# Kernel tuning notes

Measured on AMD Instinct MI355X. Metric: run time of the kernel, lower is better.

## Reference

```python
import jax, jax.numpy as jnp
import numpy as np

N_ENT, N_CON, DIM, R, NB = 30000, 29309, 128, 12, 8
B, LC, S, E_DB, E_CON = 256, 50, 32, 300000, 200000


def setup_inputs() -> dict:
    key = jax.random.key(0)
    ks = jax.random.split(key, 32)
    f = lambda k, sh: (jax.random.normal(k, sh, jnp.float32) * 0.02)
    concept_emb = f(ks[0], (N_CON, DIM)).at[0].set(0.0)  # padding_idx=0 row zeroed
    inp = {
        'concept_mask': jax.random.randint(ks[1], (B, LC), 0, N_CON, jnp.int32),
        'seed_pad': jax.random.randint(ks[2], (B, S), 0, N_ENT, jnp.int32),
        'seed_lens': jax.random.randint(ks[3], (B,), 0, S + 1, jnp.int32),
        'db_edge_index': jax.random.randint(ks[4], (2, E_DB), 0, N_ENT, jnp.int32),
        'db_edge_type': jax.random.randint(ks[5], (E_DB,), 0, R, jnp.int32),
        'con_edge_index': jax.random.randint(ks[6], (2, E_CON), 0, N_CON, jnp.int32),
        'db_vec': jax.random.uniform(ks[7], (B, N_ENT), jnp.float32),
        'labels': jax.random.randint(ks[8], (B,), 0, N_ENT, jnp.int64),
        'rec': jax.random.uniform(ks[9], (B,), jnp.float32),
        'concept_emb': concept_emb,
        'basis': f(ks[10], (NB, N_ENT, DIM)),
        'comp': f(ks[11], (R, NB)),
        'rgcn_root': f(ks[12], (N_ENT, DIM)),
        'rgcn_bias': jnp.zeros((DIM,), jnp.float32),
        'gcn_w': f(ks[13], (DIM, DIM)),
        'gcn_b': jnp.zeros((DIM,), jnp.float32),
        'attn_a': f(ks[14], (DIM, DIM)),
        'attn_b': f(ks[15], (DIM, 1)),
        'attn_a_db': f(ks[16], (DIM, DIM)),
        'attn_b_db': f(ks[17], (DIM, 1)),
        'user_norm_w': f(ks[18], (DIM, 2 * DIM)),
        'user_norm_b': jnp.zeros((DIM,), jnp.float32),
        'gate_norm_w': f(ks[19], (1, DIM)),
        'gate_norm_b': jnp.zeros((1,), jnp.float32),
        'info_con_w': f(ks[20], (DIM, DIM)),
        'info_con_b': jnp.zeros((DIM,), jnp.float32),
        'info_out_db_b': jnp.zeros((N_ENT,), jnp.float32),
        'output_en_b': jnp.zeros((N_ENT,), jnp.float32),
    }
    return inp


def _forward(concept_mask, seed_pad, seed_lens, db_edge_index, db_edge_type,
             con_edge_index, db_vec, labels, rec, concept_emb, basis, comp,
             rgcn_root, rgcn_bias, gcn_w, gcn_b, attn_a, attn_b, attn_a_db,
             attn_b_db, user_norm_w, user_norm_b, gate_norm_w, gate_norm_b,
             info_con_w, info_con_b, info_out_db_b, output_en_b):
    NEG = jnp.float32(-1e30)
    # ---- RGCN over DBpedia graph (x=None -> per-edge row W[rel][src]) ----
    w = jnp.einsum('rb,bnd->rnd', comp, basis)            # [R, N_ent, D]
    src, dst = db_edge_index[0], db_edge_index[1]
    msg = w[db_edge_type, src]                            # [E, D]
    agg = jax.ops.segment_sum(msg, dst, num_segments=N_ENT)
    cnt = jax.ops.segment_sum(jnp.ones_like(dst, jnp.float32), dst, num_segments=N_ENT)
    db_feats = agg / jnp.maximum(cnt, 1.0)[:, None] + rgcn_root + rgcn_bias  # mean aggr + root + bias
    # ---- GCN over concept graph (symmetric norm, self-loops) ----
    xw = concept_emb @ gcn_w
    loops = jnp.arange(N_CON, dtype=con_edge_index.dtype)
    cs = jnp.concatenate([con_edge_index[0], loops])
    cd = jnp.concatenate([con_edge_index[1], loops])
    deg = jax.ops.segment_sum(jnp.ones_like(cd, jnp.float32), cd, num_segments=N_CON)
    dinv = jnp.where(deg > 0, jax.lax.rsqrt(jnp.maximum(deg, 1e-12)), 0.0)
    norm = dinv[cs] * dinv[cd]
    con_feats = jax.ops.segment_sum(norm[:, None] * xw[cs], cd, num_segments=N_CON) + gcn_b
    # ---- per-sample seed-set self-attention over db features ----
    h = db_feats[seed_pad]                                # [B, S, D]
    e = jnp.tanh(h @ attn_a_db) @ attn_b_db               # [B, S, 1]
    valid = jnp.arange(S)[None, :] < seed_lens[:, None]   # [B, S]
    a = jax.nn.softmax(jnp.where(valid[..., None], e, NEG), axis=1)
    db_user = jnp.einsum('bso,bsd->bd', a, h)             # weighted sum (o=1)
    has_seed = (seed_lens > 0)
    db_user = jnp.where(has_seed[:, None], db_user, 0.0)  # empty seed set -> zeros
    db_con_mask = has_seed.astype(jnp.float32)
    # ---- batch self-attention over gathered concept features ----
    hc = con_feats[concept_mask]                          # [B, LC, D]
    ec = jnp.tanh(hc @ attn_a) @ attn_b                   # [B, LC, 1]
    cvalid = (concept_mask != 0)
    ac = jax.nn.softmax(jnp.where(cvalid[..., None], ec, NEG), axis=1)
    con_user = jnp.einsum('blo,bld->bd', ac, hc)
    # ---- gated fusion ----
    u = jnp.concatenate([con_user, db_user], axis=-1) @ user_norm_w.T + user_norm_b
    gate = jax.nn.sigmoid(u @ gate_norm_w.T + gate_norm_b)  # [B, 1]
    user_emb = gate * db_user + (1.0 - gate) * con_user
    entity_scores = user_emb @ db_feats.T + output_en_b   # [B, N_ent]
    # ---- infomax MSE loss ----
    con_e = con_user @ info_con_w.T + info_con_b
    db_scores = con_e @ db_feats.T + info_out_db_b
    info_db_loss = jnp.mean(jnp.sum((db_scores - db_vec) ** 2, axis=-1) * db_con_mask)
    # ---- rec CE loss ----
    logp = jax.nn.log_softmax(entity_scores, axis=-1)
    ce = -jnp.take_along_axis(logp, labels[:, None].astype(jnp.int32), axis=1)[:, 0]
    rec_loss = jnp.sum(ce * rec)
    loss = rec_loss + 0.025 * info_db_loss                # pretrain=False path
    return loss, entity_scores, rec_loss


def reference(concept_mask, seed_pad, seed_lens, db_edge_index, db_edge_type,
              con_edge_index, db_vec, labels, rec, concept_emb, basis, comp,
              rgcn_root, rgcn_bias, gcn_w, gcn_b, attn_a, attn_b, attn_a_db,
              attn_b_db, user_norm_w, user_norm_b, gate_norm_w, gate_norm_b,
              info_con_w, info_con_b, info_out_db_b, output_en_b):
    return _forward(concept_mask, seed_pad, seed_lens, db_edge_index, db_edge_type,
                    con_edge_index, db_vec, labels, rec, concept_emb, basis, comp,
                    rgcn_root, rgcn_bias, gcn_w, gcn_b, attn_a, attn_b, attn_a_db,
                    attn_b_db, user_norm_w, user_norm_b, gate_norm_w, gate_norm_b,
                    info_con_w, info_con_b, info_out_db_b, output_en_b)
```

## Files before the change

kernel.cpp:

```cpp
#include <hip/hip_runtime.h>

#define N_ENT  30000
#define N_CON  29309
#define DIM    128
#define NBASIS 8
#define NREL   12
#define BATCH  256
#define LCON   50
#define SSEED  32
#define EDB    300000
#define ECON   200000
#define NTILE  938

#define NE4      ((N_CON * DIM) / 4)
#define NB_HIST  ((EDB + ECON + 255) / 256)
#define NB_CONV  ((NE4 + (DIM*DIM/4) + 255) / 256)
#define NB_WCOMP ((N_ENT * 32) / 256)
#define NB_GXW   ((N_CON + 31) / 32)
#define NB_RG    ((N_ENT + 3) / 4)
#define NB_GG    ((N_CON + 3) / 4)

typedef __attribute__((ext_vector_type(8)))  short bfrag8;
typedef __attribute__((ext_vector_type(16))) float facc16;

__device__ __forceinline__ unsigned short f2bf(float f) {
    unsigned int u = __float_as_uint(f);
    u += 0x7FFFu + ((u >> 16) & 1u);
    return (unsigned short)(u >> 16);
}
__device__ __forceinline__ float bf2f(unsigned int h) {
    return __uint_as_float(h << 16);
}

__global__ __launch_bounds__(256) void prep_kernel(const int* __restrict__ db_dst,
                                                   const int* __restrict__ con_dst,
                                                   const float* __restrict__ emb,
                                                   const float* __restrict__ W,
                                                   int* __restrict__ cnt_e, int* __restrict__ cnt_c,
                                                   int* __restrict__ ord_db, int* __restrict__ ord_con,
                                                   unsigned short* __restrict__ emb_h,
                                                   unsigned short* __restrict__ Wt_h) {
    int t = threadIdx.x, bb = blockIdx.x;
    if (bb < NB_HIST) {
        int e = bb * 256 + t;
        if (e < EDB) {
            ord_db[e] = atomicAdd(cnt_e + db_dst[e], 1);
        } else if (e < EDB + ECON) {
            int ee = e - EDB;
            ord_con[ee] = atomicAdd(cnt_c + con_dst[ee], 1);
        }
    } else {
        int i = (bb - NB_HIST) * 256 + t;
        if (i < NE4) {
            float4 v = ((const float4*)emb)[i];
            unsigned int p0 = (unsigned int)f2bf(v.x) | ((unsigned int)f2bf(v.y) << 16);
            unsigned int p1 = (unsigned int)f2bf(v.z) | ((unsigned int)f2bf(v.w) << 16);
            *(uint2*)(emb_h + (size_t)i * 4) = make_uint2(p0, p1);
        } else {
            int j = i - NE4;
            if (j < (DIM * DIM) / 4) {
                int o = j * 4;
                int n = o >> 7, k0 = o & 127;
                unsigned int p0 = (unsigned int)f2bf(W[(k0 + 0) * DIM + n]) |
                                  ((unsigned int)f2bf(W[(k0 + 1) * DIM + n]) << 16);
                unsigned int p1 = (unsigned int)f2bf(W[(k0 + 2) * DIM + n]) |
                                  ((unsigned int)f2bf(W[(k0 + 3) * DIM + n]) << 16);
                *(uint2*)(Wt_h + n * DIM + k0) = make_uint2(p0, p1);
            }
        }
    }
}

__device__ void scan_block(const int* __restrict__ cnt, int n, int* __restrict__ rowptr) {
    __shared__ int part[1024];
    int t = threadIdx.x;
    int per = (n + 1023) / 1024;
    int s0 = t * per;
    int sum = 0;
    for (int i = 0; i < per; ++i) {
        int idx = s0 + i;
        if (idx < n) sum += cnt[idx];
    }
    part[t] = sum;
    __syncthreads();
    for (int off = 1; off < 1024; off <<= 1) {
        int v = (t >= off) ? part[t - off] : 0;
        __syncthreads();
        part[t] += v;
        __syncthreads();
    }
    int run = part[t] - sum;
    for (int i = 0; i < per; ++i) {
        int idx = s0 + i;
        if (idx < n) {
            rowptr[idx] = run;
            run += cnt[idx];
        }
    }
    if (t == 1023) rowptr[n] = part[1023];
}

__global__ __launch_bounds__(1024) void scan2_kernel(const int* __restrict__ cnt_e,
                                                     const int* __restrict__ cnt_c,
                                                     int* __restrict__ rowptr_e,
                                                     int* __restrict__ rowptr_c,
                                                     float* __restrict__ dinv) {
    if (blockIdx.x == 0) {
        scan_block(cnt_e, N_ENT, rowptr_e);
    } else {
        scan_block(cnt_c, N_CON, rowptr_c);
        for (int i = threadIdx.x; i < N_CON; i += 1024)
            dinv[i] = rsqrtf((float)(cnt_c[i] + 1));
    }
}

__global__ __launch_bounds__(256) void mid_kernel(const int* __restrict__ db_eidx,
                                                  const int* __restrict__ db_etype,
                                                  const int* __restrict__ con_eidx,
                                                  const int* __restrict__ ord_db,
                                                  const int* __restrict__ ord_con,
                                                  const int* __restrict__ rowptr_e,
                                                  const int* __restrict__ rowptr_c,
                                                  int* __restrict__ elist_e,
                                                  int* __restrict__ elist_c,
                                                  const float* __restrict__ basis,
                                                  const float* __restrict__ comp,
                                                  unsigned short* __restrict__ w_h,
                                                  const unsigned short* __restrict__ emb_h,
                                                  const unsigned short* __restrict__ Wt_h,
                                                  unsigned short* __restrict__ xw_h,
                                                  int use_w) {
    __shared__ float sc[NREL * NBASIS];
    int t = threadIdx.x, bb = blockIdx.x;
    if (bb < NB_HIST) {
        int e = bb * 256 + t;
        if (e < EDB) {
            int dst = db_eidx[EDB + e];
            elist_e[rowptr_e[dst] + ord_db[e]] = db_eidx[e] | (db_etype[e] << 18);
        } else if (e < EDB + ECON) {
            int ee = e - EDB;
            int dst = con_eidx[ECON + ee];
            elist_c[rowptr_c[dst] + ord_con[ee]] = con_eidx[ee];
        }
        return;
    }
    if (bb < NB_HIST + NB_WCOMP) {
        if (!use_w) return;
        if (t < NREL * NBASIS) sc[t] = comp[t];
        __syncthreads();
        int i = (bb - NB_HIST) * 256 + t;
        int n = i >> 5, d4 = i & 31;
        float4 bv[NBASIS];
#pragma unroll
        for (int b = 0; b < NBASIS; ++b)
            bv[b] = ((const float4*)(basis + ((size_t)b * N_ENT + n) * DIM))[d4];
#pragma unroll
        for (int r = 0; r < NREL; ++r) {
            float4 acc = make_float4(0.f, 0.f, 0.f, 0.f);
#pragma unroll
            for (int b = 0; b < NBASIS; ++b) {
                float c = sc[r * NBASIS + b];
                acc.x += c * bv[b].x; acc.y += c * bv[b].y;
                acc.z += c * bv[b].z; acc.w += c * bv[b].w;
            }
            unsigned int p0 = (unsigned int)f2bf(acc.x) | ((unsigned int)f2bf(acc.y) << 16);
            unsigned int p1 = (unsigned int)f2bf(acc.z) | ((unsigned int)f2bf(acc.w) << 16);
            *(uint2*)(w_h + ((size_t)r * N_ENT + n) * DIM + d4 * 4) = make_uint2(p0, p1);
        }
        return;
    }
    {
        int gb = bb - NB_HIST - NB_WCOMP;
        int wave = t >> 6, lane = t & 63;
        int m0 = gb * 32;
        int n0 = wave * 32;
        int am = lane & 31, ak = (lane >> 5) * 8;
        int mrow = m0 + am;
        bool mv = mrow < N_CON;
        const unsigned short* Ar = emb_h + (size_t)mrow * DIM + ak;
        const unsigned short* Br = Wt_h + (size_t)(n0 + am) * DIM + ak;
        facc16 acc;
#pragma unroll
        for (int r = 0; r < 16; ++r) acc[r] = 0.f;
#pragma unroll
        for (int s = 0; s < 8; ++s) {
            bfrag8 a;
#pragma unroll
            for (int j = 0; j < 8; ++j) a[j] = 0;
            if (mv) a = *(const bfrag8*)(Ar + s * 16);
            bfrag8 b = *(const bfrag8*)(Br + s * 16);
            acc = __builtin_amdgcn_mfma_f32_32x32x16_bf16(a, b, acc, 0, 0, 0);
        }
        int col = lane & 31;
        int g4 = (lane >> 5) * 4;
#pragma unroll
        for (int r = 0; r < 16; ++r) {
            int m = m0 + (r & 3) + ((r >> 2) << 3) + g4;
            if (m < N_CON) xw_h[(size_t)m * DIM + n0 + col] = f2bf(acc[r]);
        }
    }
}

__global__ __launch_bounds__(256) void gathers_kernel(const int* __restrict__ rowptr_e,
                                                      const int* __restrict__ elist_e,
                                                      const unsigned short* __restrict__ w_h,
                                                      const float* __restrict__ root,
                                                      const float* __restrict__ bias,
                                                      unsigned short* __restrict__ dbf_h,
                                                      const int* __restrict__ rowptr_c,
                                                      const int* __restrict__ elist_c,
                                                      const float* __restrict__ dinv,
                                                      const unsigned short* __restrict__ xw_h,
                                                      const float* __restrict__ gcn_b,
                                                      unsigned short* __restrict__ conf_h) {
    int bb = blockIdx.x;
    int lane = threadIdx.x & 63;
    if (bb < NB_RG) {
        int wid = bb * 4 + (threadIdx.x >> 6);
        if (wid >= N_ENT) return;
        int beg = rowptr_e[wid], end = rowptr_e[wid + 1];
        float a0 = 0.f, a1 = 0.f;
        int p = beg;
        for (; p + 1 < end; p += 2) {
            int v0 = elist_e[p], v1 = elist_e[p + 1];
            unsigned int k0 = *(const unsigned int*)(w_h + ((size_t)(v0 >> 18) * N_ENT + (v0 & 0x3FFFF)) * DIM + lane * 2);
            unsigned int k1 = *(const unsigned int*)(w_h + ((size_t)(v1 >> 18) * N_ENT + (v1 & 0x3FFFF)) * DIM + lane * 2);
            a0 += bf2f(k0 & 0xFFFF) + bf2f(k1 & 0xFFFF);
            a1 += bf2f(k0 >> 16)    + bf2f(k1 >> 16);
        }
        if (p < end) {
            int v = elist_e[p];
            unsigned int k = *(const unsigned int*)(w_h + ((size_t)(v >> 18) * N_ENT + (v & 0x3FFFF)) * DIM + lane * 2);
            a0 += bf2f(k & 0xFFFF);
            a1 += bf2f(k >> 16);
        }
        float inv = 1.f / fmaxf((float)(end - beg), 1.f);
        size_t base = (size_t)wid * DIM + lane * 2;
        float f0 = a0 * inv + root[base]     + bias[lane * 2];
        float f1 = a1 * inv + root[base + 1] + bias[lane * 2 + 1];
        *(unsigned int*)(dbf_h + base) = (unsigned int)f2bf(f0) | ((unsigned int)f2bf(f1) << 16);
    } else {
        int wid = (bb - NB_RG) * 4 + (threadIdx.x >> 6);
        if (wid >= N_CON) return;
        int beg = rowptr_c[wid], end = rowptr_c[wid + 1];
        float a0 = 0.f, a1 = 0.f;
        int p = beg;
        for (; p + 1 < end; p += 2) {
            int s0 = elist_c[p], s1 = elist_c[p + 1];
            float n0 = dinv[s0], n1 = dinv[s1];
            unsigned int k0 = *(const unsigned int*)(xw_h + (size_t)s0 * DIM + lane * 2);
            unsigned int k1 = *(const unsigned int*)(xw_h + (size_t)s1 * DIM + lane * 2);
            a0 += n0 * bf2f(k0 & 0xFFFF) + n1 * bf2f(k1 & 0xFFFF);
            a1 += n0 * bf2f(k0 >> 16)    + n1 * bf2f(k1 >> 16);
        }
        if (p < end) {
            int s = elist_c[p];
            float nm = dinv[s];
            unsigned int k = *(const unsigned int*)(xw_h + (size_t)s * DIM + lane * 2);
            a0 += nm * bf2f(k & 0xFFFF);
            a1 += nm * bf2f(k >> 16);
        }
        float dv = dinv[wid];
        unsigned int ks = *(const unsigned int*)(xw_h + (size_t)wid * DIM + lane * 2);
        size_t base = (size_t)wid * DIM + lane * 2;
        float f0 = dv * a0 + dv * dv * bf2f(ks & 0xFFFF) + gcn_b[lane * 2];
        float f1 = dv * a1 + dv * dv * bf2f(ks >> 16)    + gcn_b[lane * 2 + 1];
        *(unsigned int*)(conf_h + base) = (unsigned int)f2bf(f0) | ((unsigned int)f2bf(f1) << 16);
    }
}

__global__ __launch_bounds__(256) void rgcn_gather_basis(const int* __restrict__ rowptr,
                                                         const int* __restrict__ elist,
                                                         const float* __restrict__ basis,
                                                         const float* __restrict__ comp,
                                                         const float* __restrict__ root,
                                                         const float* __restrict__ bias,
                                                         unsigned short* __restrict__ dbf_h) {
    int wid  = blockIdx.x * 4 + (threadIdx.x >> 6);
    int lane = threadIdx.x & 63;
    if (wid >= N_ENT) return;
    int beg = rowptr[wid], end = rowptr[wid + 1];
    float a0 = 0.f, a1 = 0.f;
    for (int p = beg; p < end; ++p) {
        int v = elist[p];
        int src = v & 0x3FFFF, ty = v >> 18;
        const float* c = comp + ty * NBASIS;
#pragma unroll
        for (int b = 0; b < NBASIS; ++b) {
            const float* bp = basis + ((size_t)b * N_ENT + src) * DIM;
            a0 += c[b] * bp[lane * 2];
            a1 += c[b] * bp[lane * 2 + 1];
        }
    }
    float inv = 1.f / fmaxf((float)(end - beg), 1.f);
    size_t base = (size_t)wid * DIM + lane * 2;
    float f0 = a0 * inv + root[base]     + bias[lane * 2];
    float f1 = a1 * inv + root[base + 1] + bias[lane * 2 + 1];
    *(unsigned int*)(dbf_h + base) = (unsigned int)f2bf(f0) | ((unsigned int)f2bf(f1) << 16);
}

__device__ void attn_phase(const unsigned short* __restrict__ feats_h,
                           const int* __restrict__ row,
                           const float* __restrict__ A,
                           const float* __restrict__ vvec,
                           float* __restrict__ h, float* __restrict__ sc,
                           float* __restrict__ outv, int S, int len, int mode) {
    int t = threadIdx.x;
    for (int i = t; i < S * (DIM / 2); i += 256) {
        int s = i >> 6, d2 = (i & 63) * 2;
        unsigned int k = *(const unsigned int*)(feats_h + (size_t)row[s] * DIM + d2);
        h[(s << 7) + d2]     = bf2f(k & 0xFFFF);
        h[(s << 7) + d2 + 1] = bf2f(k >> 16);
    }
    if (t < S) sc[t] = 0.f;
    __syncthreads();
    for (int sd = t; sd < S * DIM; sd += 256) {
        int s = sd >> 7, d = sd & 127;
        float acc = 0.f;
        for (int k = 0; k < DIM; ++k) acc += h[(s << 7) + k] * A[(k << 7) + d];
        atomicAdd(&sc[s], tanhf(acc) * vvec[d]);
    }
    __syncthreads();
    if (t == 0) {
        float m = -1e30f;
        for (int s = 0; s < S; ++s) {
            bool valid = (mode == 0) ? (s < len) : (row[s] != 0);
            float e = valid ? sc[s] : -1e30f;
            sc[s] = e;
            m = fmaxf(m, e);
        }
        float sum = 0.f;
        for (int s = 0; s < S; ++s) { float p = __expf(sc[s] - m); sum += p; sc[s] = p; }
        float inv = 1.f / sum;
        for (int s = 0; s < S; ++s) sc[s] *= inv;
    }
    __syncthreads();
    if (t < DIM) {
        float acc = 0.f;
        for (int s = 0; s < S; ++s) acc += sc[s] * h[(s << 7) + t];
        if (mode == 0 && len == 0) acc = 0.f;
        outv[t] = acc;
    }
    __syncthreads();
}

__global__ __launch_bounds__(256) void attn_fusion_kernel(const unsigned short* __restrict__ dbf_h,
                                                          const unsigned short* __restrict__ conf_h,
                                                          const int* __restrict__ seed_pad,
                                                          const int* __restrict__ seed_lens,
                                                          const int* __restrict__ concept_mask,
                                                          const float* __restrict__ A_db, const float* __restrict__ v_db,
                                                          const float* __restrict__ A_c,  const float* __restrict__ v_c,
                                                          const float* __restrict__ Wu, const float* __restrict__ bu,
                                                          const float* __restrict__ gw, const float* __restrict__ gb,
                                                          const float* __restrict__ Wi, const float* __restrict__ bi,
                                                          unsigned short* __restrict__ uemb_h,
                                                          unsigned short* __restrict__ cone_h,
                                                          float* __restrict__ maskv) {
    __shared__ float h[LCON * DIM];
    __shared__ float sc[LCON];
    __shared__ float du[DIM], cu[DIM], red[DIM];
    int b = blockIdx.x, t = threadIdx.x;
    int len = seed_lens[b];
    attn_phase(dbf_h, seed_pad + b * SSEED, A_db, v_db, h, sc, du, SSEED, len, 0);
    attn_phase(conf_h, concept_mask + b * LCON, A_c, v_c, h, sc, cu, LCON, 0, 1);
    if (t < DIM) {
        float u = bu[t];
        const float* wr = Wu + t * 2 * DIM;
        for (int k = 0; k < DIM; ++k) u += cu[k] * wr[k];
        for (int k = 0; k < DIM; ++k) u += du[k] * wr[DIM + k];
        red[t] = u * gw[t];
    }
    __syncthreads();
    for (int s2 = 64; s2 > 0; s2 >>= 1) {
        if (t < s2) red[t] += red[t + s2];
        __syncthreads();
    }
    if (t < DIM) {
        float gate = 1.f / (1.f + __expf(-(red[0] + gb[0])));
        uemb_h[b * DIM + t] = f2bf(gate * du[t] + (1.f - gate) * cu[t]);
        float ce = bi[t];
        const float* wi = Wi + t * DIM;
        for (int k = 0; k < DIM; ++k) ce += cu[k] * wi[k];
        cone_h[b * DIM + t] = f2bf(ce);
    }
    if (t == 0) maskv[b] = (len > 0) ? 1.f : 0.f;
}

__global__ __launch_bounds__(256) void score_mfma(const unsigned short* __restrict__ dbf_h,
                                                  const unsigned short* __restrict__ uemb_h,
                                                  const unsigned short* __restrict__ cone_h,
                                                  const float* __restrict__ en_b,
                                                  const float* __restrict__ info_b,
                                                  const float* __restrict__ db_vec,
                                                  float* __restrict__ escore,
                                                  float* __restrict__ partM,
                                                  float* __restrict__ partS,
                                                  float* __restrict__ partQ) {
    int wave = threadIdx.x >> 6, lane = threadIdx.x & 63;
    int nt = blockIdx.x * 4 + wave;
    if (nt >= NTILE) return;
    int b0 = blockIdx.y * 32;
    int n0 = nt * 32;
    int am = lane & 31, ak = (lane >> 5) * 8;
    int nb = n0 + am;
    bool bvalid = nb < N_ENT;
    const unsigned short* Au = uemb_h + (size_t)(b0 + am) * DIM + ak;
    const unsigned short* Ac = cone_h + (size_t)(b0 + am) * DIM + ak;
    const unsigned short* Bp = dbf_h + (size_t)nb * DIM + ak;
    facc16 accE, accD;
#pragma unroll
    for (int r = 0; r < 16; ++r) { accE[r] = 0.f; accD[r] = 0.f; }
#pragma unroll
    for (int s = 0; s < 8; ++s) {
        bfrag8 au = *(const bfrag8*)(Au + s * 16);
        bfrag8 ac = *(const bfrag8*)(Ac + s * 16);
        bfrag8 bb;
#pragma unroll
        for (int j = 0; j < 8; ++j) bb[j] = 0;
        if (bvalid) bb = *(const bfrag8*)(Bp + s * 16);
        accE = __builtin_amdgcn_mfma_f32_32x32x16_bf16(au, bb, accE, 0, 0, 0);
        accD = __builtin_amdgcn_mfma_f32_32x32x16_bf16(ac, bb, accD, 0, 0, 0);
    }
    int col = lane & 31;
    int n = n0 + col;
    bool nv = n < N_ENT;
    float enb = nv ? en_b[n] : 0.f;
    float inb = nv ? info_b[n] : 0.f;
    int g4 = (lane >> 5) * 4;
#pragma unroll
    for (int r = 0; r < 16; ++r) {
        int b = b0 + (r & 3) + ((r >> 2) << 3) + g4;
        float e = accE[r] + enb;
        if (nv) escore[(size_t)b * N_ENT + n] = e;
        float ev = nv ? e : -1e30f;
        float mx = ev;
#pragma unroll
        for (int off = 16; off >= 1; off >>= 1) mx = fmaxf(mx, __shfl_xor(mx, off, 64));
        float ex = nv ? __expf(e - mx) : 0.f;
        float sm = ex;
#pragma unroll
        for (int off = 16; off >= 1; off >>= 1) sm += __shfl_xor(sm, off, 64);
        float d = nv ? (accD[r] + inb - db_vec[(size_t)b * N_ENT + n]) : 0.f;
        float q = d * d;
#pragma unroll
        for (int off = 16; off >= 1; off >>= 1) q += __shfl_xor(q, off, 64);
        if (col == 0) {
            partM[(size_t)b * NTILE + nt] = mx;
            partS[(size_t)b * NTILE + nt] = sm;
            partQ[(size_t)b * NTILE + nt] = q;
        }
    }
}

__global__ __launch_bounds__(256) void ce_final(const float* __restrict__ partM,
                                                const float* __restrict__ partS,
                                                const float* __restrict__ partQ,
                                                const float* __restrict__ escore,
                                                const int* __restrict__ labels,
                                                const float* __restrict__ rec,
                                                float* __restrict__ rloss,
                                                float* __restrict__ ssqv) {
    __shared__ float red[256], red2[256];
    int b = blockIdx.x, t = threadIdx.x;
    const float* pm = partM + (size_t)b * NTILE;
    const float* ps = partS + (size_t)b * NTILE;
    const float* pq = partQ + (size_t)b * NTILE;
    float mx = -1e30f;
    for (int i = t; i < NTILE; i += 256) mx = fmaxf(mx, pm[i]);
    red[t] = mx;
    __syncthreads();
    for (int s2 = 128; s2 > 0; s2 >>= 1) {
        if (t < s2) red[t] = fmaxf(red[t], red[t + s2]);
        __syncthreads();
    }
    float M = red[0];
    __syncthreads();
    float s = 0.f, q = 0.f;
    for (int i = t; i < NTILE; i += 256) {
        s += ps[i] * __expf(pm[i] - M);
        q += pq[i];
    }
    red[t] = s; red2[t] = q;
    __syncthreads();
    for (int s2 = 128; s2 > 0; s2 >>= 1) {
        if (t < s2) { red[t] += red[t + s2]; red2[t] += red2[t + s2]; }
        __syncthreads();
    }
    if (t == 0) {
        float lse = M + logf(red[0]);
        float ce  = -(escore[(size_t)b * N_ENT + labels[b]] - lse);
        rloss[b]  = ce * rec[b];
        ssqv[b]   = red2[0];
    }
}

__global__ __launch_bounds__(256) void final_kernel(const float* __restrict__ rloss,
                                                    const float* __restrict__ sumsq,
                                                    const float* __restrict__ maskv,
                                                    float* __restrict__ out) {
    __shared__ float r1[256], r2[256];
    int t = threadIdx.x;
    r1[t] = rloss[t];
    r2[t] = sumsq[t] * maskv[t];
    __syncthreads();
    for (int s2 = 128; s2 > 0; s2 >>= 1) {
        if (t < s2) { r1[t] += r1[t + s2]; r2[t] += r2[t + s2]; }
        __syncthreads();
    }
    if (t == 0) {
        float rec_loss = r1[0];
        float info = r2[0] / (float)BATCH;
        out[0] = rec_loss + 0.025f * info;
        out[1 + (size_t)BATCH * N_ENT] = rec_loss;
    }
}

extern "C" void kernel_launch(void* const* d_in, const int* in_sizes, int n_in,
                              void* d_out, int out_size, void* d_ws, size_t ws_size,
                              hipStream_t stream) {
    (void)in_sizes; (void)n_in; (void)out_size;
    const int*   concept_mask  = (const int*)d_in[0];
    const int*   seed_pad      = (const int*)d_in[1];
    const int*   seed_lens     = (const int*)d_in[2];
    const int*   db_eidx       = (const int*)d_in[3];
    const int*   db_etype      = (const int*)d_in[4];
    const int*   con_eidx      = (const int*)d_in[5];
    const float* db_vec        = (const float*)d_in[6];
    const int*   labels        = (const int*)d_in[7];
    const float* rec           = (const float*)d_in[8];
    const float* concept_emb   = (const float*)d_in[9];
    const float* basis         = (const float*)d_in[10];
    const float* comp          = (const float*)d_in[11];
    const float* rgcn_root     = (const float*)d_in[12];
    const float* rgcn_bias     = (const float*)d_in[13];
    const float* gcn_w         = (const float*)d_in[14];
    const float* gcn_b         = (const float*)d_in[15];
    const float* attn_a        = (const float*)d_in[16];
    const float* attn_b        = (const float*)d_in[17];
    const float* attn_a_db     = (const float*)d_in[18];
    const float* attn_b_db     = (const float*)d_in[19];
    const float* user_norm_w   = (const float*)d_in[20];
    const float* user_norm_b   = (const float*)d_in[21];
    const float* gate_norm_w   = (const float*)d_in[22];
    const float* gate_norm_b   = (const float*)d_in[23];
    const float* info_con_w    = (const float*)d_in[24];
    const float* info_con_b    = (const float*)d_in[25];
    const float* info_out_db_b = (const float*)d_in[26];
    const float* output_en_b   = (const float*)d_in[27];

    float* ws = (float*)d_ws;
    size_t off = 0;
    auto alloc = [&](size_t n) { float* p = ws + off; off += (n + 255) & ~(size_t)255; return p; };
    float* dinv   = alloc(N_CON);
    float* maskv  = alloc(BATCH);
    float* rls    = alloc(BATCH);
    float* ssqv   = alloc(BATCH);
    float* partM  = alloc((size_t)BATCH * NTILE);
    float* partS  = alloc((size_t)BATCH * NTILE);
    float* partQ  = alloc((size_t)BATCH * NTILE);
    int* cnt_e    = (int*)alloc(N_ENT + N_CON);
    int* cnt_c    = cnt_e + N_ENT;
    int* rowptr_e = (int*)alloc(N_ENT + 1);
    int* rowptr_c = (int*)alloc(N_CON + 1);
    int* ord_db   = (int*)alloc(EDB);
    int* ord_con  = (int*)alloc(ECON);
    int* elist_e  = (int*)alloc(EDB);
    int* elist_c  = (int*)alloc(ECON);
    unsigned short* dbf_h  = (unsigned short*)alloc((size_t)N_ENT * DIM / 2);
    unsigned short* conf_h = (unsigned short*)alloc((size_t)N_CON * DIM / 2 + 128);
    unsigned short* xw_h   = (unsigned short*)alloc((size_t)N_CON * DIM / 2 + 128);
    unsigned short* emb_h  = (unsigned short*)alloc((size_t)N_CON * DIM / 2 + 128);
    unsigned short* Wt_h   = (unsigned short*)alloc(DIM * DIM / 2);
    unsigned short* uemb_h = (unsigned short*)alloc(BATCH * DIM / 2);
    unsigned short* cone_h = (unsigned short*)alloc(BATCH * DIM / 2);
    size_t w_elems = ((size_t)NREL * N_ENT * DIM) / 2;
    int use_w = (off + w_elems) * sizeof(float) <= ws_size;
    unsigned short* w_h = (unsigned short*)(ws + off);

    float* out    = (float*)d_out;
    float* escore = out + 1;

    (void)hipMemsetAsync(cnt_e, 0, (N_ENT + N_CON) * sizeof(int), stream);

    prep_kernel<<<NB_HIST + NB_CONV, 256, 0, stream>>>(db_eidx + EDB, con_eidx + ECON,
                                                       concept_emb, gcn_w,
                                                       cnt_e, cnt_c, ord_db, ord_con, emb_h, Wt_h);
    scan2_kernel<<<2, 1024, 0, stream>>>(cnt_e, cnt_c, rowptr_e, rowptr_c, dinv);
    mid_kernel<<<NB_HIST + NB_WCOMP + NB_GXW, 256, 0, stream>>>(db_eidx, db_etype, con_eidx,
                                                                ord_db, ord_con, rowptr_e, rowptr_c,
                                                                elist_e, elist_c, basis, comp, w_h,
                                                                emb_h, Wt_h, xw_h, use_w);
    gathers_kernel<<<NB_RG + NB_GG, 256, 0, stream>>>(rowptr_e, elist_e, w_h, rgcn_root, rgcn_bias,
                                                      dbf_h, rowptr_c, elist_c, dinv, xw_h, gcn_b, conf_h);
    if (!use_w) {
        rgcn_gather_basis<<<NB_RG, 256, 0, stream>>>(rowptr_e, elist_e, basis, comp,
                                                     rgcn_root, rgcn_bias, dbf_h);
    }
    attn_fusion_kernel<<<BATCH, 256, 0, stream>>>(dbf_h, conf_h, seed_pad, seed_lens, concept_mask,
                                                  attn_a_db, attn_b_db, attn_a, attn_b,
                                                  user_norm_w, user_norm_b, gate_norm_w, gate_norm_b,
                                                  info_con_w, info_con_b, uemb_h, cone_h, maskv);
    dim3 sg((NTILE + 3) / 4, BATCH / 32);
    score_mfma<<<sg, 256, 0, stream>>>(dbf_h, uemb_h, cone_h, output_en_b, info_out_db_b, db_vec,
                                       escore, partM, partS, partQ);
    ce_final<<<BATCH, 256, 0, stream>>>(partM, partS, partQ, escore, labels, rec, rls, ssqv);
    final_kernel<<<1, 256, 0, stream>>>(rls, ssqv, maskv, out);
}
```

Measured before the change: 591.7 us.

## Precompute per-entity attention scores with MFMA and simplify attention fusion to gathers

The attention logit tanh(h·A)·v depends only on the entity row, not on the batch. It is now computed once for every entity and concept row in a new bf16 MFMA kernel, instead of being recomputed per batch element with scalar FP32 loops over 32 and 50 gathered rows. The attention-fusion kernel then only gathers these scalar scores, runs a wave-level softmax, and does the weighted sum. This removes the per-batch serial matmul and atomics. In exchange it computes scores for all ~59k rows whether or not they are referenced, and it uses bf16 inputs for the attention matrices.

```diff
diff --git a/kernel.cpp b/kernel.cpp
--- a/kernel.cpp
+++ b/kernel.cpp
@@ -14,11 +14,13 @@
 
 #define NE4      ((N_CON * DIM) / 4)
 #define NB_HIST  ((EDB + ECON + 255) / 256)
-#define NB_CONV  ((NE4 + (DIM*DIM/4) + 255) / 256)
+#define NB_CONV  ((NE4 + 3 * (DIM * DIM / 4) + 255) / 256)
 #define NB_WCOMP ((N_ENT * 32) / 256)
 #define NB_GXW   ((N_CON + 31) / 32)
 #define NB_RG    ((N_ENT + 3) / 4)
 #define NB_GG    ((N_CON + 3) / 4)
+#define NB_EDB   ((N_ENT + 31) / 32)
+#define NB_ECON  ((N_CON + 31) / 32)
 
 typedef __attribute__((ext_vector_type(8)))  short bfrag8;
 typedef __attribute__((ext_vector_type(16))) float facc16;
@@ -36,10 +38,14 @@
                                                    const int* __restrict__ con_dst,
                                                    const float* __restrict__ emb,
                                                    const float* __restrict__ W,
+                                                   const float* __restrict__ A_db,
+                                                   const float* __restrict__ A_c,
                                                    int* __restrict__ cnt_e, int* __restrict__ cnt_c,
                                                    int* __restrict__ ord_db, int* __restrict__ ord_con,
                                                    unsigned short* __restrict__ emb_h,
-                                                   unsigned short* __restrict__ Wt_h) {
+                                                   unsigned short* __restrict__ Wt_h,
+                                                   unsigned short* __restrict__ At_db_h,
+                                                   unsigned short* __restrict__ At_c_h) {
     int t = threadIdx.x, bb = blockIdx.x;
     if (bb < NB_HIST) {
         int e = bb * 256 + t;
@@ -58,14 +64,18 @@
             *(uint2*)(emb_h + (size_t)i * 4) = make_uint2(p0, p1);
         } else {
             int j = i - NE4;
-            if (j < (DIM * DIM) / 4) {
-                int o = j * 4;
+            if (j < 3 * (DIM * DIM) / 4) {
+                int sel = j >> 12;
+                int jj = j & 4095;
+                const float* S = (sel == 0) ? W : ((sel == 1) ? A_db : A_c);
+                unsigned short* Dst = (sel == 0) ? Wt_h : ((sel == 1) ? At_db_h : At_c_h);
+                int o = jj * 4;
                 int n = o >> 7, k0 = o & 127;
-                unsigned int p0 = (unsigned int)f2bf(W[(k0 + 0) * DIM + n]) |
-                                  ((unsigned int)f2bf(W[(k0 + 1) * DIM + n]) << 16);
-                unsigned int p1 = (unsigned int)f2bf(W[(k0 + 2) * DIM + n]) |
-                                  ((unsigned int)f2bf(W[(k0 + 3) * DIM + n]) << 16);
-                *(uint2*)(Wt_h + n * DIM + k0) = make_uint2(p0, p1);
+                unsigned int p0 = (unsigned int)f2bf(S[(k0 + 0) * DIM + n]) |
+                                  ((unsigned int)f2bf(S[(k0 + 1) * DIM + n]) << 16);
+                unsigned int p1 = (unsigned int)f2bf(S[(k0 + 2) * DIM + n]) |
+                                  ((unsigned int)f2bf(S[(k0 + 3) * DIM + n]) << 16);
+                *(uint2*)(Dst + n * DIM + k0) = make_uint2(p0, p1);
             }
         }
     }
@@ -299,71 +309,132 @@
     *(unsigned int*)(dbf_h + base) = (unsigned int)f2bf(f0) | ((unsigned int)f2bf(f1) << 16);
 }
 
-__device__ void attn_phase(const unsigned short* __restrict__ feats_h,
-                           const int* __restrict__ row,
-                           const float* __restrict__ A,
-                           const float* __restrict__ vvec,
-                           float* __restrict__ h, float* __restrict__ sc,
-                           float* __restrict__ outv, int S, int len, int mode) {
-    int t = threadIdx.x;
-    for (int i = t; i < S * (DIM / 2); i += 256) {
-        int s = i >> 6, d2 = (i & 63) * 2;
-        unsigned int k = *(const unsigned int*)(feats_h + (size_t)row[s] * DIM + d2);
-        h[(s << 7) + d2]     = bf2f(k & 0xFFFF);
-        h[(s << 7) + d2 + 1] = bf2f(k >> 16);
-    }
-    if (t < S) sc[t] = 0.f;
-    __syncthreads();
-    for (int sd = t; sd < S * DIM; sd += 256) {
-        int s = sd >> 7, d = sd & 127;
-        float acc = 0.f;
-        for (int k = 0; k < DIM; ++k) acc += h[(s << 7) + k] * A[(k << 7) + d];
-        atomicAdd(&sc[s], tanhf(acc) * vvec[d]);
-    }
-    __syncthreads();
-    if (t == 0) {
-        float m = -1e30f;
-        for (int s = 0; s < S; ++s) {
-            bool valid = (mode == 0) ? (s < len) : (row[s] != 0);
-            float e = valid ? sc[s] : -1e30f;
-            sc[s] = e;
-            m = fmaxf(m, e);
-        }
-        float sum = 0.f;
-        for (int s = 0; s < S; ++s) { float p = __expf(sc[s] - m); sum += p; sc[s] = p; }
-        float inv = 1.f / sum;
-        for (int s = 0; s < S; ++s) sc[s] *= inv;
-    }
-    __syncthreads();
-    if (t < DIM) {
-        float acc = 0.f;
-        for (int s = 0; s < S; ++s) acc += sc[s] * h[(s << 7) + t];
-        if (mode == 0 && len == 0) acc = 0.f;
-        outv[t] = acc;
-    }
-    __syncthreads();
+__global__ __launch_bounds__(256) void escore_kernel(const unsigned short* __restrict__ dbf_h,
+                                                     const unsigned short* __restrict__ conf_h,
+                                                     const unsigned short* __restrict__ At_db_h,
+                                                     const float* __restrict__ v_db,
+                                                     const unsigned short* __restrict__ At_c_h,
+                                                     const float* __restrict__ v_c,
+                                                     float* __restrict__ e_db,
+                                                     float* __restrict__ e_con) {
+    __shared__ float part[4][32];
+    int t = threadIdx.x, bb = blockIdx.x;
+    int wave = t >> 6, lane = t & 63;
+    const unsigned short* feats;
+    const unsigned short* At;
+    const float* v;
+    float* eo;
+    int m0, nrow;
+    if (bb < NB_EDB) {
+        feats = dbf_h;  At = At_db_h; v = v_db; eo = e_db;  m0 = bb * 32;             nrow = N_ENT;
+    } else {
+        feats = conf_h; At = At_c_h;  v = v_c;  eo = e_con; m0 = (bb - NB_EDB) * 32;  nrow = N_CON;
+    }
+    int n0 = wave * 32;
+    int am = lane & 31, ak = (lane >> 5) * 8;
+    int mrow = m0 + am;
+    bool mv = mrow < nrow;
+    const unsigned short* Ar = feats + (size_t)mrow * DIM + ak;
+    const unsigned short* Br = At + (size_t)(n0 + am) * DIM + ak;
+    facc16 acc;
+#pragma unroll
+    for (int r = 0; r < 16; ++r) acc[r] = 0.f;
+#pragma unroll
+    for (int s = 0; s < 8; ++s) {
+        bfrag8 a;
+#pragma unroll
+        for (int j = 0; j < 8; ++j) a[j] = 0;
+        if (mv) a = *(const bfrag8*)(Ar + s * 16);
+        bfrag8 b = *(const bfrag8*)(Br + s * 16);
+        acc = __builtin_amdgcn_mfma_f32_32x32x16_bf16(a, b, acc, 0, 0, 0);
+    }
+    int col = lane & 31, g = lane >> 5;
+    float vn = v[n0 + col];
+#pragma unroll
+    for (int r = 0; r < 16; ++r) {
+        float x = tanhf(acc[r]) * vn;
+#pragma unroll
+        for (int off = 16; off >= 1; off >>= 1) x += __shfl_xor(x, off, 32);
+        if (col == 0) {
+            int row = (r & 3) + ((r >> 2) << 3) + (g << 2);
+            part[wave][row] = x;
+        }
+    }
+    __syncthreads();
+    if (t < 32) {
+        int m = m0 + t;
+        if (m < nrow)
+            eo[m] = part[0][t] + part[1][t] + part[2][t] + part[3][t];
+    }
 }
 
 __global__ __launch_bounds__(256) void attn_fusion_kernel(const unsigned short* __restrict__ dbf_h,
                                                           const unsigned short* __restrict__ conf_h,
+                                                          const float* __restrict__ e_db,
+                                                          const float* __restrict__ e_con,
                                                           const int* __restrict__ seed_pad,
                                                           const int* __restrict__ seed_lens,
                                                           const int* __restrict__ concept_mask,
-                                                          const float* __restrict__ A_db, const float* __restrict__ v_db,
-                                                          const float* __restrict__ A_c,  const float* __restrict__ v_c,
                                                           const float* __restrict__ Wu, const float* __restrict__ bu,
                                                           const float* __restrict__ gw, const float* __restrict__ gb,
                                                           const float* __restrict__ Wi, const float* __restrict__ bi,
                                                           unsigned short* __restrict__ uemb_h,
                                                           unsigned short* __restrict__ cone_h,
                                                           float* __restrict__ maskv) {
-    __shared__ float h[LCON * DIM];
-    __shared__ float sc[LCON];
+    __shared__ int srow[SSEED];
+    __shared__ int crow[LCON];
+    __shared__ float a_db[SSEED], a_con[LCON];
     __shared__ float du[DIM], cu[DIM], red[DIM];
     int b = blockIdx.x, t = threadIdx.x;
+    int wave = t >> 6, lane = t & 63;
     int len = seed_lens[b];
-    attn_phase(dbf_h, seed_pad + b * SSEED, A_db, v_db, h, sc, du, SSEED, len, 0);
-    attn_phase(conf_h, concept_mask + b * LCON, A_c, v_c, h, sc, cu, LCON, 0, 1);
+    if (wave == 0) {
+        float e = -1e30f;
+        if (lane < SSEED) {
+            int rv = seed_pad[b * SSEED + lane];
+            srow[lane] = rv;
+            if (lane < len) e = e_db[rv];
+        }
+        float m = e;
+#pragma unroll
+        for (int off = 16; off >= 1; off >>= 1) m = fmaxf(m, __shfl_xor(m, off, 32));
+        float p = (lane < SSEED) ? __expf(e - m) : 0.f;
+        float s = p;
+#pragma unroll
+        for (int off = 16; off >= 1; off >>= 1) s += __shfl_xor(s, off, 32);
+        if (lane < SSEED) a_db[lane] = p / s;
+    } else if (wave == 1) {
+        float e = -1e30f;
+        if (lane < LCON) {
+            int rv = concept_mask[b * LCON + lane];
+            crow[lane] = rv;
+            if (rv != 0) e = e_con[rv];
+        }
+        float m = e;
+#pragma unroll
+        for (int off = 32; off >= 1; off >>= 1) m = fmaxf(m, __shfl_xor(m, off, 64));
+        float p = (lane < LCON) ? __expf(e - m) : 0.f;
+        float s = p;
+#pragma unroll
+        for (int off = 32; off >= 1; off >>= 1) s += __shfl_xor(s, off, 64);
+        if (lane < LCON) a_con[lane] = p / s;
+    }
+    __syncthreads();
+    if (t < DIM) {
+        float acc = 0.f;
+#pragma unroll
+        for (int s = 0; s < SSEED; ++s)
+            acc += a_db[s] * bf2f((unsigned int)dbf_h[(size_t)srow[s] * DIM + t]);
+        du[t] = (len > 0) ? acc : 0.f;
+    } else {
+        int d = t - DIM;
+        float acc = 0.f;
+#pragma unroll
+        for (int s = 0; s < LCON; ++s)
+            acc += a_con[s] * bf2f((unsigned int)conf_h[(size_t)crow[s] * DIM + d]);
+        cu[d] = acc;
+    }
+    __syncthreads();
     if (t < DIM) {
         float u = bu[t];
         const float* wr = Wu + t * 2 * DIM;
@@ -574,6 +645,10 @@
     unsigned short* Wt_h   = (unsigned short*)alloc(DIM * DIM / 2);
     unsigned short* uemb_h = (unsigned short*)alloc(BATCH * DIM / 2);
     unsigned short* cone_h = (unsigned short*)alloc(BATCH * DIM / 2);
+    float* e_db   = alloc(N_ENT);
+    float* e_con  = alloc(N_CON);
+    unsigned short* At_db_h = (unsigned short*)alloc(DIM * DIM / 2);
+    unsigned short* At_c_h  = (unsigned short*)alloc(DIM * DIM / 2);
     size_t w_elems = ((size_t)NREL * N_ENT * DIM) / 2;
     int use_w = (off + w_elems) * sizeof(float) <= ws_size;
     unsigned short* w_h = (unsigned short*)(ws + off);
@@ -584,8 +659,9 @@
     (void)hipMemsetAsync(cnt_e, 0, (N_ENT + N_CON) * sizeof(int), stream);
 
     prep_kernel<<<NB_HIST + NB_CONV, 256, 0, stream>>>(db_eidx + EDB, con_eidx + ECON,
-                                                       concept_emb, gcn_w,
-                                                       cnt_e, cnt_c, ord_db, ord_con, emb_h, Wt_h);
+                                                       concept_emb, gcn_w, attn_a_db, attn_a,
+                                                       cnt_e, cnt_c, ord_db, ord_con, emb_h, Wt_h,
+                                                       At_db_h, At_c_h);
     scan2_kernel<<<2, 1024, 0, stream>>>(cnt_e, cnt_c, rowptr_e, rowptr_c, dinv);
     mid_kernel<<<NB_HIST + NB_WCOMP + NB_GXW, 256, 0, stream>>>(db_eidx, db_etype, con_eidx,
                                                                 ord_db, ord_con, rowptr_e, rowptr_c,
@@ -597,8 +673,10 @@
         rgcn_gather_basis<<<NB_RG, 256, 0, stream>>>(rowptr_e, elist_e, basis, comp,
                                                      rgcn_root, rgcn_bias, dbf_h);
     }
-    attn_fusion_kernel<<<BATCH, 256, 0, stream>>>(dbf_h, conf_h, seed_pad, seed_lens, concept_mask,
-                                                  attn_a_db, attn_b_db, attn_a, attn_b,
+    escore_kernel<<<NB_EDB + NB_ECON, 256, 0, stream>>>(dbf_h, conf_h, At_db_h, attn_b_db,
+                                                        At_c_h, attn_b, e_db, e_con);
+    attn_fusion_kernel<<<BATCH, 256, 0, stream>>>(dbf_h, conf_h, e_db, e_con,
+                                                  seed_pad, seed_lens, concept_mask,
                                                   user_norm_w, user_norm_b, gate_norm_w, gate_norm_b,
                                                   info_con_w, info_con_b, uemb_h, cone_h, maskv);
     dim3 sg((NTILE + 3) / 4, BATCH / 32);
```

Result: faster. 526.7 us (-11.0%).
